# Performance work log

Hardware: AMD Instinct MI355X
Metric: run time of the kernel (lower is better)

The kernel has to match this reference:

```python
import jax, jax.numpy as jnp
import numpy as np

N_USER = 50_000
N_ITEM = 100_000
N = N_USER + N_ITEM          # total graph nodes
E = 2_400_000                # nnz of normalized adjacency (avg degree ~16)
D = 64                       # emb_size; layers = [64, 64, 64]
SLOPE = 0.2                  # NGCF uses LeakyReLU(alpha=0.2)


def setup_inputs() -> dict:
    key = jax.random.key(0)
    ks = jax.random.split(key, 20)
    inp = {
        "user_emb": jax.random.normal(ks[0], (N_USER, D), jnp.float32) * 0.1,
        "item_emb": jax.random.normal(ks[1], (N_ITEM, D), jnp.float32) * 0.1,
    }
    for k in range(3):
        inp[f"W_gc_{k}"] = jax.random.normal(ks[2 + 4 * k], (D, D), jnp.float32) * 0.1
        inp[f"b_gc_{k}"] = jax.random.normal(ks[3 + 4 * k], (1, D), jnp.float32) * 0.1
        inp[f"W_bi_{k}"] = jax.random.normal(ks[4 + 4 * k], (D, D), jnp.float32) * 0.1
        inp[f"b_bi_{k}"] = jax.random.normal(ks[5 + 4 * k], (1, D), jnp.float32) * 0.1
    inp["adj_vals"] = jax.random.uniform(ks[14], (E,), jnp.float32) * (1.0 / 16.0)
    inp["adj_rows"] = jax.random.randint(ks[15], (E,), 0, N, jnp.int32)
    inp["adj_cols"] = jax.random.randint(ks[16], (E,), 0, N, jnp.int32)
    return inp


def _l2norm(x):
    n = jnp.linalg.norm(x, axis=1, keepdims=True)
    return x / jnp.maximum(n, 1e-12)


def reference(user_emb, item_emb,
              W_gc_0, b_gc_0, W_bi_0, b_bi_0,
              W_gc_1, b_gc_1, W_bi_1, b_bi_1,
              W_gc_2, b_gc_2, W_bi_2, b_bi_2,
              adj_vals, adj_rows, adj_cols):
    Wg = [W_gc_0, W_gc_1, W_gc_2]
    bg = [b_gc_0, b_gc_1, b_gc_2]
    Wb = [W_bi_0, W_bi_1, W_bi_2]
    bb = [b_bi_0, b_bi_1, b_bi_2]

    ego = jnp.concatenate([user_emb, item_emb], axis=0)  # [N, D]
    all_embs = [ego]
    for k in range(3):
        # side = norm_adj @ ego  (sparse COO spmm via gather + segment_sum)
        msgs = adj_vals[:, None] * ego[adj_cols]          # [E, D]
        side = jax.ops.segment_sum(msgs, adj_rows, num_segments=N)
        sum_emb = jax.nn.leaky_relu(side @ Wg[k] + bg[k], SLOPE)
        bi_emb = jax.nn.leaky_relu((ego * side) @ Wb[k] + bb[k], SLOPE)
        ego = sum_emb + bi_emb
        all_embs.append(_l2norm(ego))
    return jnp.concatenate(all_embs, axis=1)              # [N, 4*D]
```

## Files before the change

### kernel.cpp

```cpp
#include <hip/hip_runtime.h>

#define N_TOT      150000
#define N_USER     50000
#define N_EDGE     2400000
#define DIM        64
#define OUT_STRIDE 256
#define SLOPE      0.2f
#define NB_SCAN    ((N_TOT + 255) / 256)


__global__ void init_ego(const float* __restrict__ ue, const float* __restrict__ ie,
                         float* __restrict__ ego, float* __restrict__ out) {
    int idx = blockIdx.x * blockDim.x + threadIdx.x;
    if (idx >= N_TOT * DIM / 4) return;
    int n  = idx >> 4;
    int c4 = idx & 15;
    float4 v = (n < N_USER) ? ((const float4*)ue)[idx]
                            : ((const float4*)ie)[idx - N_USER * (DIM / 4)];
    ((float4*)ego)[idx] = v;
    ((float4*)out)[n * (OUT_STRIDE / 4) + c4] = v;
}

__global__ void hist_rows(const int* __restrict__ rows, int* __restrict__ cnt) {
    int e = blockIdx.x * blockDim.x + threadIdx.x;
    if (e >= N_EDGE) return;
    atomicAdd(&cnt[rows[e]], 1);
}

__global__ __launch_bounds__(256) void scan_partial(const int* __restrict__ cnt,
                                                    int* __restrict__ row_ptr,
                                                    int* __restrict__ bsum) {
    __shared__ int s[256];
    int tid = threadIdx.x;
    int i = blockIdx.x * 256 + tid;
    int v = (i < N_TOT) ? cnt[i] : 0;
    s[tid] = v;
    __syncthreads();
    for (int off = 1; off < 256; off <<= 1) {
        int t = (tid >= off) ? s[tid - off] : 0;
        __syncthreads();
        s[tid] += t;
        __syncthreads();
    }
    if (i < N_TOT) row_ptr[i] = s[tid] - v;
    if (tid == 255) bsum[blockIdx.x] = s[255];
}

__global__ __launch_bounds__(1024) void scan_bsums(int* __restrict__ bsum) {
    __shared__ int s[1024];
    int tid = threadIdx.x;
    int v = (tid < NB_SCAN) ? bsum[tid] : 0;
    s[tid] = v;
    __syncthreads();
    for (int off = 1; off < 1024; off <<= 1) {
        int t = (tid >= off) ? s[tid - off] : 0;
        __syncthreads();
        s[tid] += t;
        __syncthreads();
    }
    if (tid < NB_SCAN) bsum[tid] = s[tid] - v;
}

__global__ __launch_bounds__(256) void add_offsets(int* __restrict__ row_ptr,
                                                   const int* __restrict__ bsum,
                                                   int* __restrict__ cursor) {
    int i = blockIdx.x * 256 + threadIdx.x;
    if (i < N_TOT) {
        int v = row_ptr[i] + bsum[blockIdx.x];
        row_ptr[i] = v;
        cursor[i]  = v;
    }
    if (i == 0) row_ptr[N_TOT] = N_EDGE;
}

__global__ void scatter_edges(const int* __restrict__ rows, const int* __restrict__ cols,
                              const float* __restrict__ vals, int* __restrict__ cursor,
                              int2* __restrict__ epack) {
    int e = blockIdx.x * blockDim.x + threadIdx.x;
    if (e >= N_EDGE) return;
    int r = rows[e];
    int pos = atomicAdd(&cursor[r], 1);
    epack[pos] = make_int2(cols[e], __float_as_int(vals[e]));
}

__global__ __launch_bounds__(256) void spmm_gather(
    const int* __restrict__ row_ptr, const int2* __restrict__ epack,
    const float* __restrict__ ego, float* __restrict__ side) {
    int lane = threadIdx.x & 63;
    int row  = blockIdx.x * 4 + (threadIdx.x >> 6);
    if (row >= N_TOT) return;
    int beg = row_ptr[row];
    int end = row_ptr[row + 1];
    float sv = 0.f;
    int i = beg;
    for (; i + 4 <= end; i += 4) {
        int2 e0 = epack[i + 0];
        int2 e1 = epack[i + 1];
        int2 e2 = epack[i + 2];
        int2 e3 = epack[i + 3];
        float g0 = ego[(size_t)e0.x * DIM + lane];
        float g1 = ego[(size_t)e1.x * DIM + lane];
        float g2 = ego[(size_t)e2.x * DIM + lane];
        float g3 = ego[(size_t)e3.x * DIM + lane];
        sv = fmaf(__int_as_float(e0.y), g0, sv);
        sv = fmaf(__int_as_float(e1.y), g1, sv);
        sv = fmaf(__int_as_float(e2.y), g2, sv);
        sv = fmaf(__int_as_float(e3.y), g3, sv);
    }
    for (; i < end; ++i) {
        int2 e = epack[i];
        sv = fmaf(__int_as_float(e.y), ego[(size_t)e.x * DIM + lane], sv);
    }
    side[(size_t)row * DIM + lane] = sv;
}

__global__ __launch_bounds__(256) void transform_gemm(
    const float* __restrict__ Wg, const float* __restrict__ bgv,
    const float* __restrict__ Wb, const float* __restrict__ bbv,
    const float* __restrict__ side, float* __restrict__ ego,
    float* __restrict__ out, int layer) {
    __shared__ float sST[DIM][68];
    __shared__ float sPT[DIM][68];
    __shared__ float sWg[DIM][DIM];
    __shared__ float sWb[DIM][DIM];
    int tid = threadIdx.x;
    int R0  = blockIdx.x * 64;

    #pragma unroll
    for (int it = 0; it < 4; ++it) {
        int f = tid + it * 256;
        float4 wg = ((const float4*)Wg)[f];
        float4 wb = ((const float4*)Wb)[f];
        int k = f >> 4, c = (f & 15) * 4;
        *(float4*)&sWg[k][c] = wg;
        *(float4*)&sWb[k][c] = wb;
    }
    #pragma unroll
    for (int it = 0; it < 4; ++it) {
        int f  = tid + it * 256;
        int r  = f >> 4, k0 = (f & 15) * 4;
        int row = R0 + r;
        float4 s4 = make_float4(0.f, 0.f, 0.f, 0.f);
        float4 e4 = make_float4(0.f, 0.f, 0.f, 0.f);
        if (row < N_TOT) {
            s4 = *(const float4*)&side[(size_t)row * DIM + k0];
            e4 = *(const float4*)&ego [(size_t)row * DIM + k0];
        }
        sST[k0 + 0][r] = s4.x; sST[k0 + 1][r] = s4.y;
        sST[k0 + 2][r] = s4.z; sST[k0 + 3][r] = s4.w;
        sPT[k0 + 0][r] = s4.x * e4.x; sPT[k0 + 1][r] = s4.y * e4.y;
        sPT[k0 + 2][r] = s4.z * e4.z; sPT[k0 + 3][r] = s4.w * e4.w;
    }
    __syncthreads();

    int tx = tid & 15, ty = tid >> 4;
    int c0 = tx * 4, r0 = ty * 4;
    float ag[4][4] = {{0.f}}, ab[4][4] = {{0.f}};
    #pragma unroll 4
    for (int k = 0; k < DIM; ++k) {
        float4 s4 = *(const float4*)&sST[k][r0];
        float4 p4 = *(const float4*)&sPT[k][r0];
        float4 g4 = *(const float4*)&sWg[k][c0];
        float4 b4 = *(const float4*)&sWb[k][c0];
        float ss[4] = {s4.x, s4.y, s4.z, s4.w};
        float pp[4] = {p4.x, p4.y, p4.z, p4.w};
        float gg[4] = {g4.x, g4.y, g4.z, g4.w};
        float bw[4] = {b4.x, b4.y, b4.z, b4.w};
        #pragma unroll
        for (int i = 0; i < 4; ++i)
            #pragma unroll
            for (int j = 0; j < 4; ++j) {
                ag[i][j] = fmaf(ss[i], gg[j], ag[i][j]);
                ab[i][j] = fmaf(pp[i], bw[j], ab[i][j]);
            }
    }

    float4 bg4 = *(const float4*)&bgv[c0];
    float4 bb4 = *(const float4*)&bbv[c0];
    float bgl[4] = {bg4.x, bg4.y, bg4.z, bg4.w};
    float bbl[4] = {bb4.x, bb4.y, bb4.z, bb4.w};

    float ne[4][4];
    float ss2[4];
    #pragma unroll
    for (int i = 0; i < 4; ++i) {
        float s = 0.f;
        #pragma unroll
        for (int j = 0; j < 4; ++j) {
            float g = ag[i][j] + bgl[j];
            float b = ab[i][j] + bbl[j];
            g = g > 0.f ? g : SLOPE * g;
            b = b > 0.f ? b : SLOPE * b;
            float v = g + b;
            ne[i][j] = v;
            s = fmaf(v, v, s);
        }
        ss2[i] = s;
    }
    #pragma unroll
    for (int m = 1; m < 16; m <<= 1) {
        #pragma unroll
        for (int i = 0; i < 4; ++i) ss2[i] += __shfl_xor(ss2[i], m, 64);
    }

    float* outbase = out + (size_t)(layer + 1) * DIM;
    #pragma unroll
    for (int i = 0; i < 4; ++i) {
        int row = R0 + r0 + i;
        if (row >= N_TOT) break;
        float inv = 1.f / fmaxf(sqrtf(ss2[i]), 1e-12f);
        float4 e4 = make_float4(ne[i][0], ne[i][1], ne[i][2], ne[i][3]);
        float4 o4 = make_float4(ne[i][0] * inv, ne[i][1] * inv, ne[i][2] * inv, ne[i][3] * inv);
        *(float4*)&ego[(size_t)row * DIM + c0] = e4;
        *(float4*)&outbase[(size_t)row * OUT_STRIDE + c0] = o4;
    }
}

extern "C" void kernel_launch(void* const* d_in, const int* in_sizes, int n_in,
                              void* d_out, int out_size, void* d_ws, size_t ws_size,
                              hipStream_t stream) {
    const float* ue = (const float*)d_in[0];
    const float* ie = (const float*)d_in[1];
    const float* Wg[3] = {(const float*)d_in[2], (const float*)d_in[6], (const float*)d_in[10]};
    const float* bg[3] = {(const float*)d_in[3], (const float*)d_in[7], (const float*)d_in[11]};
    const float* Wb[3] = {(const float*)d_in[4], (const float*)d_in[8], (const float*)d_in[12]};
    const float* bb[3] = {(const float*)d_in[5], (const float*)d_in[9], (const float*)d_in[13]};
    const float* vals = (const float*)d_in[14];
    const int*  rows  = (const int*)d_in[15];
    const int*  cols  = (const int*)d_in[16];
    float* out = (float*)d_out;

    float* ego     = (float*)d_ws;
    float* side    = ego + (size_t)N_TOT * DIM;
    int2*  epack   = (int2*)(side + (size_t)N_TOT * DIM);
    int*   row_ptr = (int*)(epack + N_EDGE);
    int*   cursor  = row_ptr + (N_TOT + 16);
    int*   bsum    = cursor + N_TOT;

    hipMemsetAsync(cursor, 0, (size_t)N_TOT * sizeof(int), stream);
    hist_rows<<<(N_EDGE + 255) / 256, 256, 0, stream>>>(rows, cursor);
    scan_partial<<<NB_SCAN, 256, 0, stream>>>(cursor, row_ptr, bsum);
    scan_bsums<<<1, 1024, 0, stream>>>(bsum);
    add_offsets<<<NB_SCAN, 256, 0, stream>>>(row_ptr, bsum, cursor);
    scatter_edges<<<(N_EDGE + 255) / 256, 256, 0, stream>>>(rows, cols, vals, cursor, epack);

    init_ego<<<(N_TOT * DIM / 4 + 255) / 256, 256, 0, stream>>>(ue, ie, ego, out);

    for (int k = 0; k < 3; ++k) {
        spmm_gather<<<(N_TOT + 3) / 4, 256, 0, stream>>>(row_ptr, epack, ego, side);
        transform_gemm<<<(N_TOT + 63) / 64, 256, 0, stream>>>(Wg[k], bg[k], Wb[k], bb[k],
                                                              side, ego, out, k);
    }
}
```

Measured before the change: 963.1 us.

## Capture edge ranks during histogram and vectorize SpMM gather with float4 lanes

The histogram kernel now records each edge's atomic rank, so the scatter pass computes positions from row_ptr plus rank instead of doing a second round of atomics. Both kernels process four edges per thread with int4/float4 loads. The SpMM gather splits each wavefront into four 16-lane groups, each handling a different edge with float4 loads, then combines the groups with cross-lane shuffles. This should raise memory-level parallelism for short rows, at the cost of extra shuffle reductions and reusing the side buffer as rank storage.

```diff
diff --git a/kernel.cpp b/kernel.cpp
--- a/kernel.cpp
+++ b/kernel.cpp
@@ -21,10 +21,17 @@
     ((float4*)out)[n * (OUT_STRIDE / 4) + c4] = v;
 }
 
-__global__ void hist_rows(const int* __restrict__ rows, int* __restrict__ cnt) {
-    int e = blockIdx.x * blockDim.x + threadIdx.x;
-    if (e >= N_EDGE) return;
-    atomicAdd(&cnt[rows[e]], 1);
+__global__ void hist_rank(const int* __restrict__ rows, int* __restrict__ cnt,
+                          int* __restrict__ rank) {
+    int t = blockIdx.x * blockDim.x + threadIdx.x;
+    if (t >= N_EDGE / 4) return;
+    int4 r4 = ((const int4*)rows)[t];
+    int4 k4;
+    k4.x = atomicAdd(&cnt[r4.x], 1);
+    k4.y = atomicAdd(&cnt[r4.y], 1);
+    k4.z = atomicAdd(&cnt[r4.z], 1);
+    k4.w = atomicAdd(&cnt[r4.w], 1);
+    ((int4*)rank)[t] = k4;
 }
 
 __global__ __launch_bounds__(256) void scan_partial(const int* __restrict__ cnt,
@@ -62,25 +69,26 @@
 }
 
 __global__ __launch_bounds__(256) void add_offsets(int* __restrict__ row_ptr,
-                                                   const int* __restrict__ bsum,
-                                                   int* __restrict__ cursor) {
+                                                   const int* __restrict__ bsum) {
     int i = blockIdx.x * 256 + threadIdx.x;
-    if (i < N_TOT) {
-        int v = row_ptr[i] + bsum[blockIdx.x];
-        row_ptr[i] = v;
-        cursor[i]  = v;
-    }
+    if (i < N_TOT) row_ptr[i] += bsum[blockIdx.x];
     if (i == 0) row_ptr[N_TOT] = N_EDGE;
 }
 
 __global__ void scatter_edges(const int* __restrict__ rows, const int* __restrict__ cols,
-                              const float* __restrict__ vals, int* __restrict__ cursor,
-                              int2* __restrict__ epack) {
-    int e = blockIdx.x * blockDim.x + threadIdx.x;
-    if (e >= N_EDGE) return;
-    int r = rows[e];
-    int pos = atomicAdd(&cursor[r], 1);
-    epack[pos] = make_int2(cols[e], __float_as_int(vals[e]));
+                              const float* __restrict__ vals,
+                              const int* __restrict__ row_ptr,
+                              const int* __restrict__ rank, int2* __restrict__ epack) {
+    int t = blockIdx.x * blockDim.x + threadIdx.x;
+    if (t >= N_EDGE / 4) return;
+    int4   r4 = ((const int4*)rows)[t];
+    int4   k4 = ((const int4*)rank)[t];
+    int4   c4 = ((const int4*)cols)[t];
+    float4 v4 = ((const float4*)vals)[t];
+    epack[row_ptr[r4.x] + k4.x] = make_int2(c4.x, __float_as_int(v4.x));
+    epack[row_ptr[r4.y] + k4.y] = make_int2(c4.y, __float_as_int(v4.y));
+    epack[row_ptr[r4.z] + k4.z] = make_int2(c4.z, __float_as_int(v4.z));
+    epack[row_ptr[r4.w] + k4.w] = make_int2(c4.w, __float_as_int(v4.w));
 }
 
 __global__ __launch_bounds__(256) void spmm_gather(
@@ -91,27 +99,36 @@
     if (row >= N_TOT) return;
     int beg = row_ptr[row];
     int end = row_ptr[row + 1];
-    float sv = 0.f;
+    int g = lane >> 4;
+    int q = lane & 15;
+    float4 acc = make_float4(0.f, 0.f, 0.f, 0.f);
     int i = beg;
-    for (; i + 4 <= end; i += 4) {
-        int2 e0 = epack[i + 0];
-        int2 e1 = epack[i + 1];
-        int2 e2 = epack[i + 2];
-        int2 e3 = epack[i + 3];
-        float g0 = ego[(size_t)e0.x * DIM + lane];
-        float g1 = ego[(size_t)e1.x * DIM + lane];
-        float g2 = ego[(size_t)e2.x * DIM + lane];
-        float g3 = ego[(size_t)e3.x * DIM + lane];
-        sv = fmaf(__int_as_float(e0.y), g0, sv);
-        sv = fmaf(__int_as_float(e1.y), g1, sv);
-        sv = fmaf(__int_as_float(e2.y), g2, sv);
-        sv = fmaf(__int_as_float(e3.y), g3, sv);
-    }
-    for (; i < end; ++i) {
-        int2 e = epack[i];
-        sv = fmaf(__int_as_float(e.y), ego[(size_t)e.x * DIM + lane], sv);
-    }
-    side[(size_t)row * DIM + lane] = sv;
+    for (; i + 8 <= end; i += 8) {
+        int4 ee = ((const int4*)(epack + i))[g];
+        float4 va = ((const float4*)(ego + (size_t)ee.x * DIM))[q];
+        float4 vb = ((const float4*)(ego + (size_t)ee.z * DIM))[q];
+        float wa = __int_as_float(ee.y);
+        float wb = __int_as_float(ee.w);
+        acc.x = fmaf(wa, va.x, acc.x); acc.y = fmaf(wa, va.y, acc.y);
+        acc.z = fmaf(wa, va.z, acc.z); acc.w = fmaf(wa, va.w, acc.w);
+        acc.x = fmaf(wb, vb.x, acc.x); acc.y = fmaf(wb, vb.y, acc.y);
+        acc.z = fmaf(wb, vb.z, acc.z); acc.w = fmaf(wb, vb.w, acc.w);
+    }
+    for (; i < end; i += 4) {
+        if (i + g < end) {
+            int2 e = epack[i + g];
+            float4 v = ((const float4*)(ego + (size_t)e.x * DIM))[q];
+            float w = __int_as_float(e.y);
+            acc.x = fmaf(w, v.x, acc.x); acc.y = fmaf(w, v.y, acc.y);
+            acc.z = fmaf(w, v.z, acc.z); acc.w = fmaf(w, v.w, acc.w);
+        }
+    }
+    acc.x += __shfl_xor(acc.x, 16, 64); acc.y += __shfl_xor(acc.y, 16, 64);
+    acc.z += __shfl_xor(acc.z, 16, 64); acc.w += __shfl_xor(acc.w, 16, 64);
+    acc.x += __shfl_xor(acc.x, 32, 64); acc.y += __shfl_xor(acc.y, 32, 64);
+    acc.z += __shfl_xor(acc.z, 32, 64); acc.w += __shfl_xor(acc.w, 32, 64);
+    if (g == 0)
+        *(float4*)(side + (size_t)row * DIM + q * 4) = acc;
 }
 
 __global__ __launch_bounds__(256) void transform_gemm(
@@ -234,15 +251,17 @@
     float* side    = ego + (size_t)N_TOT * DIM;
     int2*  epack   = (int2*)(side + (size_t)N_TOT * DIM);
     int*   row_ptr = (int*)(epack + N_EDGE);
-    int*   cursor  = row_ptr + (N_TOT + 16);
-    int*   bsum    = cursor + N_TOT;
-
-    hipMemsetAsync(cursor, 0, (size_t)N_TOT * sizeof(int), stream);
-    hist_rows<<<(N_EDGE + 255) / 256, 256, 0, stream>>>(rows, cursor);
-    scan_partial<<<NB_SCAN, 256, 0, stream>>>(cursor, row_ptr, bsum);
+    int*   cnt     = row_ptr + (N_TOT + 16);
+    int*   bsum    = cnt + N_TOT;
+    int*   rank    = (int*)side;
+
+    hipMemsetAsync(cnt, 0, (size_t)N_TOT * sizeof(int), stream);
+    hist_rank<<<(N_EDGE / 4 + 255) / 256, 256, 0, stream>>>(rows, cnt, rank);
+    scan_partial<<<NB_SCAN, 256, 0, stream>>>(cnt, row_ptr, bsum);
     scan_bsums<<<1, 1024, 0, stream>>>(bsum);
-    add_offsets<<<NB_SCAN, 256, 0, stream>>>(row_ptr, bsum, cursor);
-    scatter_edges<<<(N_EDGE + 255) / 256, 256, 0, stream>>>(rows, cols, vals, cursor, epack);
+    add_offsets<<<NB_SCAN, 256, 0, stream>>>(row_ptr, bsum);
+    scatter_edges<<<(N_EDGE / 4 + 255) / 256, 256, 0, stream>>>(rows, cols, vals,
+                                                                row_ptr, rank, epack);
 
     init_ego<<<(N_TOT * DIM / 4 + 255) / 256, 256, 0, stream>>>(ue, ie, ego, out);
 
```

Result: faster. 801.2 us (-16.8%).
